# Kernel optimization log

Hardware: AMD Instinct MI355X
Metric: run time of the kernel (lower is better)

Reference implementation:

```python
import jax, jax.numpy as jnp
import numpy as np
import math

B, S, D, H, NF = 2, 2048, 1024, 16, 4
DH = D // H


def setup_inputs() -> dict:
    key = jax.random.key(0)
    ks = jax.random.split(key, 8)
    scale = 0.01 / math.sqrt(D)  # rough attenuated-kaiming scale for projections
    return {
        "x": jax.random.normal(ks[0], (B, S, D), dtype=jnp.float32),
        "weights": jax.random.uniform(ks[1], (1, NF), dtype=jnp.float32),
        "Wq": jax.random.normal(ks[2], (D, D), dtype=jnp.float32) * scale,
        "bq": jnp.zeros((D,), dtype=jnp.float32),
        "Wk": jax.random.normal(ks[3], (D, D), dtype=jnp.float32) * scale,
        "bk": jnp.zeros((D,), dtype=jnp.float32),
        "Wv": jax.random.normal(ks[4], (D, D), dtype=jnp.float32) * scale,
        "bv": jnp.zeros((D,), dtype=jnp.float32),
        "Wout": jax.random.normal(ks[5], (NF, D, D), dtype=jnp.float32) / math.sqrt(D),
        "bout": jnp.zeros((NF, D), dtype=jnp.float32),
    }


def reference(x, weights, Wq, bq, Wk, bk, Wv, bv, Wout, bout):
    # projections (torch Linear: x @ W.T + b)
    q = x @ Wq.T + bq  # [B,S,D]
    k = x @ Wk.T + bk
    v = x @ Wv.T + bv
    # split heads -> [B,H,S,DH]
    split = lambda t: t.reshape(B, S, H, DH).transpose(0, 2, 1, 3)
    q, k, v = split(q), split(k), split(v)
    # scores with causal additive mask of -10000 (as in get_attention_mask)
    scores = jnp.einsum("bhqd,bhkd->bhqk", q, k) / math.sqrt(DH)
    i = jnp.arange(S)
    causal = (i[None, :] <= i[:, None])  # [S,S] True where allowed
    mask = (1.0 - causal.astype(scores.dtype)) * -10000.0
    attn = jax.nn.softmax(scores + mask, axis=-1)
    # dropout is disabled (p=0.0)
    out = jnp.einsum("bhqk,bhkd->bhqd", attn, v)  # [B,H,S,DH]
    out = out.transpose(0, 2, 1, 3).reshape(B, S, D)
    # WeightedFunctions: per-function Linear(d,d) combined by weights[0]
    w0 = weights[0]  # [NF]
    Weff = jnp.einsum("f,fod->od", w0, Wout)  # [D,D]
    beff = w0 @ bout  # [D]
    return out @ Weff.T + beff
```

## Files before the change

### kernel.cpp

```cpp
#include <hip/hip_runtime.h>

typedef unsigned short u16;
typedef __bf16 bf16_t;
typedef bf16_t bf16x8 __attribute__((ext_vector_type(8)));
typedef bf16_t bf16x4 __attribute__((ext_vector_type(4)));
typedef float f32x4 __attribute__((ext_vector_type(4)));
typedef u16 u16x8 __attribute__((ext_vector_type(8)));
typedef u16 u16x4 __attribute__((ext_vector_type(4)));

#define DEV __device__ __forceinline__

DEV u16 f2bf(float f) {
  unsigned u = __float_as_uint(f);
  u += 0x7FFFu + ((u >> 16) & 1u);
  return (u16)(u >> 16);
}

DEV void async_ld16(const void* g, void* lds_wave_uniform) {
  __builtin_amdgcn_global_load_lds(
      (const __attribute__((address_space(1))) void*)g,
      (__attribute__((address_space(3))) void*)lds_wave_uniform, 16, 0, 0);
}

DEV int KF(int r) { return (r & 3) ^ ((r >> 2) & 1); }

__global__ __launch_bounds__(256) void prep_kernel(
    const float* __restrict__ x, const float* __restrict__ Wq,
    const float* __restrict__ Wk, const float* __restrict__ Wv,
    const float* __restrict__ w4, const float* __restrict__ Wout,
    const float* __restrict__ bout, u16* __restrict__ xbf,
    u16* __restrict__ wqkv, u16* __restrict__ Weff, float* __restrict__ beff) {
  constexpr int NX = 1048576;
  constexpr int NW = 262144;
  const int stride = gridDim.x * 256;
  for (int id = blockIdx.x * 256 + threadIdx.x; id < NX + 3 * NW + NW;
       id += stride) {
    if (id < NX) {
      const float4 v = ((const float4*)x)[id];
      u16x4 o;
      o[0] = f2bf(v.x); o[1] = f2bf(v.y); o[2] = f2bf(v.z); o[3] = f2bf(v.w);
      ((u16x4*)xbf)[id] = o;
    } else if (id < NX + 3 * NW) {
      const int wi = id - NX;
      const int which = wi >> 18, j = wi & (NW - 1);
      const float* src = which == 0 ? Wq : (which == 1 ? Wk : Wv);
      const float4 v = ((const float4*)src)[j];
      u16x4 o;
      o[0] = f2bf(v.x); o[1] = f2bf(v.y); o[2] = f2bf(v.z); o[3] = f2bf(v.w);
      ((u16x4*)wqkv)[wi] = o;
    } else {
      const int i = id - NX - 3 * NW;
      const float w0 = w4[0], w1 = w4[1], w2 = w4[2], w3 = w4[3];
      const float4* W = (const float4*)Wout;
      const float4 a = W[i], b1 = W[NW + i], b2 = W[2 * NW + i],
                   b3 = W[3 * NW + i];
      u16x4 o;
      o[0] = f2bf(w0 * a.x + w1 * b1.x + w2 * b2.x + w3 * b3.x);
      o[1] = f2bf(w0 * a.y + w1 * b1.y + w2 * b2.y + w3 * b3.y);
      o[2] = f2bf(w0 * a.z + w1 * b1.z + w2 * b2.z + w3 * b3.z);
      o[3] = f2bf(w0 * a.w + w1 * b1.w + w2 * b2.w + w3 * b3.w);
      ((u16x4*)Weff)[i] = o;
      if (i < 256) {
        const float4* B4 = (const float4*)bout;
        const float4 ba = B4[i], c1 = B4[256 + i], c2 = B4[512 + i],
                     c3 = B4[768 + i];
        float4 ob;
        ob.x = w0 * ba.x + w1 * c1.x + w2 * c2.x + w3 * c3.x;
        ob.y = w0 * ba.y + w1 * c1.y + w2 * c2.y + w3 * c3.y;
        ob.z = w0 * ba.z + w1 * c1.z + w2 * c2.z + w3 * c3.z;
        ob.w = w0 * ba.w + w1 * c1.w + w2 * c2.w + w3 * c3.w;
        ((float4*)beff)[i] = ob;
      }
    }
  }
}

#define GEMM_PIPELINE_LOOP(A_, B_, m0_, n0_, K_)                               \
  int rA[2], oA[2], dstc[2];                                                   \
  _Pragma("unroll") for (int j = 0; j < 2; ++j) {                              \
    const int c = (j * 4 + w) * 64 + lane;                                     \
    rA[j] = c >> 2;                                                            \
    oA[j] = ((c & 3) ^ KF(rA[j])) * 8;                                         \
    dstc[j] = (j * 4 + w) * 512;                                               \
  }                                                                            \
  auto stage = [&](int buf, int kt) {                                          \
    _Pragma("unroll") for (int j = 0; j < 2; ++j) {                            \
      async_ld16(A_ + (m0_ + rA[j]) * K_ + kt + oA[j],                         \
                 &LDS[buf * 4096 + dstc[j]]);                                  \
      async_ld16(B_ + (n0_ + rA[j]) * K_ + kt + oA[j],                         \
                 &LDS[12288 + buf * 4096 + dstc[j]]);                          \
    }                                                                          \
  };                                                                           \
  f32x4 acc[4][4] = {};                                                        \
  stage(0, 0);                                                                 \
  stage(1, 32);                                                                \
  const int nt = K_ / 32;                                                      \
  int cur = 0, stg = 2;                                                        \
  for (int t = 0; t < nt; ++t) {                                               \
    if (t == nt - 1)                                                           \
      asm volatile("s_waitcnt vmcnt(0)\ns_barrier" ::: "memory");              \
    else                                                                       \
      asm volatile("s_waitcnt vmcnt(4)\ns_barrier" ::: "memory");              \
    __builtin_amdgcn_sched_barrier(0);                                         \
    if (t + 2 < nt) stage(stg, (t + 2) * 32);                                  \
    bf16x8 af[4], bfr[4];                                                      \
    _Pragma("unroll") for (int i = 0; i < 4; ++i) {                            \
      const int ra = wr * 64 + i * 16 + l15;                                   \
      const int rb = wc * 64 + i * 16 + l15;                                   \
      af[i] = *(const bf16x8*)&LDS[cur * 4096 + ra * 32 + ((l4 ^ KF(ra)) * 8)];\
      bfr[i] = *(const bf16x8*)&LDS[12288 + cur * 4096 + rb * 32 +             \
                                    ((l4 ^ KF(rb)) * 8)];                      \
    }                                                                          \
    asm volatile("s_waitcnt lgkmcnt(0)" ::: "memory");                         \
    __builtin_amdgcn_sched_barrier(0);                                         \
    __builtin_amdgcn_s_setprio(1);                                             \
    _Pragma("unroll") for (int i = 0; i < 4; ++i)                              \
        _Pragma("unroll") for (int j = 0; j < 4; ++j)                          \
            acc[i][j] = __builtin_amdgcn_mfma_f32_16x16x32_bf16(               \
                af[i], bfr[j], acc[i][j], 0, 0, 0);                            \
    __builtin_amdgcn_s_setprio(0);                                             \
    cur = cur == 2 ? 0 : cur + 1;                                              \
    stg = stg == 2 ? 0 : stg + 1;                                              \
  }

__global__ __launch_bounds__(256) void gemm_bt_kernel(
    const u16* __restrict__ A, const u16* __restrict__ Bw,
    const float* __restrict__ bias, float* __restrict__ C, int M, int N, int K) {
  __shared__ u16 LDS[24576];
  const int tid = threadIdx.x;
  const int w = tid >> 6, lane = tid & 63;
  const int l15 = lane & 15, l4 = lane >> 4;
  const int wr = w >> 1, wc = w & 1;
  const long m0 = (long)blockIdx.y * 128, n0 = (long)blockIdx.x * 128;

  GEMM_PIPELINE_LOOP(A, Bw, m0, n0, K)

#pragma unroll
  for (int i = 0; i < 4; ++i) {
    const long row0 = m0 + wr * 64 + i * 16 + l4 * 4;
#pragma unroll
    for (int j = 0; j < 4; ++j) {
      const long col = n0 + wc * 64 + j * 16 + l15;
      const float bb = bias[col];
#pragma unroll
      for (int r = 0; r < 4; ++r)
        C[(row0 + r) * N + col] = acc[i][j][r] + bb;
    }
  }
}

__global__ __launch_bounds__(256) void gemm_qkv_kernel(
    const u16* __restrict__ A, const u16* __restrict__ Bw,
    const float* __restrict__ bq, const float* __restrict__ bk,
    const float* __restrict__ bv, u16* __restrict__ qo, u16* __restrict__ ko,
    u16* __restrict__ vt) {
  constexpr int K = 1024;
  __shared__ u16 LDS[24576];
  const int tid = threadIdx.x;
  const int w = tid >> 6, lane = tid & 63;
  const int l15 = lane & 15, l4 = lane >> 4;
  const int wr = w >> 1, wc = w & 1;
  const long m0 = (long)blockIdx.y * 128, n0 = (long)blockIdx.x * 128;
  const int seg = blockIdx.x >> 3;
  const float* bias = seg == 0 ? bq : (seg == 1 ? bk : bv);
  const float scale = seg == 0 ? 0.18033688011112042f : 1.0f;

  GEMM_PIPELINE_LOOP(A, Bw, m0, n0, K)

  __syncthreads();
  const long ccol0 = n0 - (long)seg * 1024;
  if (seg < 2) {
    u16* outp = seg == 0 ? qo : ko;
#pragma unroll
    for (int i = 0; i < 4; ++i) {
#pragma unroll
      for (int j = 0; j < 4; ++j) {
        const int colb = wc * 64 + j * 16 + l15;
        const float bb = bias[ccol0 + colb];
#pragma unroll
        for (int r = 0; r < 4; ++r) {
          const int row = wr * 64 + i * 16 + l4 * 4 + r;
          LDS[row * 128 + (colb ^ ((row & 15) << 3))] =
              f2bf((acc[i][j][r] + bb) * scale);
        }
      }
    }
    __syncthreads();
#pragma unroll
    for (int p = 0; p < 8; ++p) {
      const int cid = p * 256 + tid;
      const int row = cid >> 4, c = cid & 15;
      const u16x8 vch = *(const u16x8*)&LDS[row * 128 + ((c ^ (row & 15)) * 8)];
      *(u16x8*)&outp[(m0 + row) * 1024 + ccol0 + c * 8] = vch;
    }
  } else {
    const int b = (int)(m0 >> 11);
    const int s0 = (int)(m0 & 2047);
#pragma unroll
    for (int i = 0; i < 4; ++i) {
#pragma unroll
      for (int j = 0; j < 4; ++j) {
        const int colb = wc * 64 + j * 16 + l15;
        const float bb = bias[ccol0 + colb];
#pragma unroll
        for (int r = 0; r < 4; ++r) {
          const int row = wr * 64 + i * 16 + l4 * 4 + r;
          LDS[colb * 128 + (row ^ ((colb & 15) << 3))] = f2bf(acc[i][j][r] + bb);
        }
      }
    }
    __syncthreads();
#pragma unroll
    for (int p = 0; p < 8; ++p) {
      const int cid = p * 256 + tid;
      const int c = cid >> 4, r0 = (cid & 15) * 8;
      const u16x8 vch = *(const u16x8*)&LDS[c * 128 + (r0 ^ ((c & 15) << 3))];
      const int gcol = (int)ccol0 + c;
      const int h = gcol >> 6, d = gcol & 63;
      *(u16x8*)&vt[(size_t)((b * 16 + h) * 64 + d) * 2048 + s0 + r0] = vch;
    }
  }
}

__global__ __launch_bounds__(512) void flash_kernel(
    const u16* __restrict__ Q, const u16* __restrict__ Kg,
    const u16* __restrict__ Vt, u16* __restrict__ O,
    u16* __restrict__ accP, float* __restrict__ mP, float* __restrict__ lP) {
  constexpr int S = 2048, D = 1024, DH = 64;
  __shared__ u16 Ks[3][4096];
  __shared__ u16 Vs[3][4096];
  __shared__ u16 Ps[8][2048];
  const int tid = threadIdx.x;
  const int w = tid >> 6, lane = tid & 63;
  const int l15 = lane & 15, l4 = lane >> 4;
  const int bh = blockIdx.x, b = bh >> 4, h = bh & 15;
  const int xb = blockIdx.y;
  const int p = xb >> 1, seg = xb & 1;
  const int p1len = seg ? 0 : 4 * p + 4;
  const int kvoff = seg ? (14 - 4 * p) : 0;
  const int TA = seg ? (7 - p) : p;
  const int TB = 7 - p;
  const int qbA_keep = TA * 256 + w * 32;

  const u16* Kbh = Kg + (size_t)b * S * D + h * DH;
  const u16* Vbh = Vt + (size_t)bh * DH * S;

  const int srow = tid >> 3;
  const int scol = ((tid & 7) ^ (srow & 7)) * 8;
  const int sw = l15 & 7;

  bf16x8 qf[2][2], qfB[2][2];
#pragma unroll
  for (int c = 0; c < 2; ++c) {
    const u16* qp =
        Q + (size_t)(b * S + qbA_keep + c * 16 + l15) * D + h * DH + l4 * 8;
    qf[c][0] = *(const bf16x8*)qp;
    qf[c][1] = *(const bf16x8*)(qp + 32);
    qfB[c][0] = qf[c][0];
    qfB[c][1] = qf[c][1];
  }
  if (!seg) {
    const int qbB = TB * 256 + w * 32;
#pragma unroll
    for (int c = 0; c < 2; ++c) {
      const u16* qp =
          Q + (size_t)(b * S + qbB + c * 16 + l15) * D + h * DH + l4 * 8;
      qfB[c][0] = *(const bf16x8*)qp;
      qfB[c][1] = *(const bf16x8*)(qp + 32);
    }
  }

  f32x4 acc_o[2][4] = {};
  float m_run[2] = {-3e38f, -3e38f};
  float l_run[2] = {0.f, 0.f};

  int qb = qbA_keep;
  int qt64w = TA * 4 + (w >> 1);

  auto kv_of = [&](int j) { return (j < p1len) ? j : (j - p1len + kvoff); };
  auto stage = [&](int kv, int buf) {
    async_ld16(Kbh + (size_t)(kv * 64 + srow) * D + scol, &Ks[buf][w * 512]);
    async_ld16(Vbh + (size_t)srow * S + kv * 64 + scol, &Vs[buf][w * 512]);
  };

  stage(kv_of(0), 0);
  stage(kv_of(1), 1);

  constexpr int NST = 18;
  for (int j = 0; j < NST; ++j) {
    if (j == NST - 1)
      asm volatile("s_waitcnt vmcnt(0)\ns_barrier" ::: "memory");
    else
      asm volatile("s_waitcnt vmcnt(2)\ns_barrier" ::: "memory");
    __builtin_amdgcn_sched_barrier(0);
    if (j + 2 < NST) stage(kv_of(j + 2), (j + 2) % 3);

    if (seg == 0 && j == p1len) {
      float lt[2], lq[2][4];
#pragma unroll
      for (int c = 0; c < 2; ++c) {
        float t = l_run[c];
        t += __shfl_xor(t, 16);
        t += __shfl_xor(t, 32);
        lt[c] = t;
#pragma unroll
        for (int r = 0; r < 4; ++r) lq[c][r] = __shfl(lt[c], l4 * 4 + r, 64);
      }
#pragma unroll
      for (int c = 0; c < 2; ++c)
#pragma unroll
        for (int db = 0; db < 4; ++db)
#pragma unroll
          for (int r = 0; r < 4; ++r) {
            const int row = c * 16 + l4 * 4 + r;
            const int col = db * 16 + l15;
            Ps[w][row * 64 + (col ^ ((row & 7) << 3))] =
                f2bf(acc_o[c][db][r] / lq[c][r]);
          }
      asm volatile("s_waitcnt lgkmcnt(0)" ::: "memory");
#pragma unroll
      for (int j4 = 0; j4 < 4; ++j4) {
        const int cid = j4 * 64 + lane;
        const int row = cid >> 3, c8 = cid & 7;
        const u16x8 vch =
            *(const u16x8*)&Ps[w][row * 64 + ((c8 ^ (row & 7)) * 8)];
        *(u16x8*)&O[(size_t)(b * S + qbA_keep + row) * D + h * DH + c8 * 8] =
            vch;
      }
#pragma unroll
      for (int c = 0; c < 2; ++c) {
        qf[c][0] = qfB[c][0];
        qf[c][1] = qfB[c][1];
        m_run[c] = -3e38f;
        l_run[c] = 0.f;
#pragma unroll
        for (int db = 0; db < 4; ++db) acc_o[c][db] = f32x4{0.f, 0.f, 0.f, 0.f};
      }
      qb = TB * 256 + w * 32;
      qt64w = TB * 4 + (w >> 1);
    }

    const int it = kv_of(j);
    const int buf = j % 3;
    if (it <= qt64w) {
      f32x4 accs[2][4] = {};
      __builtin_amdgcn_s_setprio(1);
#pragma unroll
      for (int cb = 0; cb < 4; ++cb) {
        const int row = cb * 16 + l15;
        const bf16x8 kf0 = *(const bf16x8*)&Ks[buf][row * 64 + ((l4 ^ sw) * 8)];
        const bf16x8 kf1 =
            *(const bf16x8*)&Ks[buf][row * 64 + (((l4 + 4) ^ sw) * 8)];
#pragma unroll
        for (int c = 0; c < 2; ++c) {
          accs[c][cb] = __builtin_amdgcn_mfma_f32_16x16x32_bf16(
              kf0, qf[c][0], accs[c][cb], 0, 0, 0);
          accs[c][cb] = __builtin_amdgcn_mfma_f32_16x16x32_bf16(
              kf1, qf[c][1], accs[c][cb], 0, 0, 0);
        }
      }
      __builtin_amdgcn_s_setprio(0);
      bf16x8 vf0[4], vf1[4];
#pragma unroll
      for (int db = 0; db < 4; ++db) {
        const int row = db * 16 + l15;
        vf0[db] = *(const bf16x8*)&Vs[buf][row * 64 + ((l4 ^ sw) * 8)];
        vf1[db] = *(const bf16x8*)&Vs[buf][row * 64 + (((l4 + 4) ^ sw) * 8)];
      }
      float mx[2] = {-3e38f, -3e38f};
      if (it == qt64w) {
#pragma unroll
        for (int c = 0; c < 2; ++c)
#pragma unroll
          for (int cb = 0; cb < 4; ++cb)
#pragma unroll
            for (int r = 0; r < 4; ++r) {
              float s_ = accs[c][cb][r];
              if (it * 64 + cb * 16 + l4 * 4 + r > qb + c * 16 + l15)
                s_ = -3e38f;
              accs[c][cb][r] = s_;
              mx[c] = fmaxf(mx[c], s_);
            }
      } else {
#pragma unroll
        for (int c = 0; c < 2; ++c)
#pragma unroll
          for (int cb = 0; cb < 4; ++cb)
#pragma unroll
            for (int r = 0; r < 4; ++r) mx[c] = fmaxf(mx[c], accs[c][cb][r]);
      }
      if (!__all(fmaxf(mx[0] - m_run[0], mx[1] - m_run[1]) <= 8.0f)) {
#pragma unroll
        for (int c = 0; c < 2; ++c) {
          float m = mx[c];
          m = fmaxf(m, __shfl_xor(m, 16));
          m = fmaxf(m, __shfl_xor(m, 32));
          const float mn = fmaxf(m_run[c], m);
          const float corr = __builtin_amdgcn_exp2f(m_run[c] - mn);
          m_run[c] = mn;
          float cq[4];
#pragma unroll
          for (int r = 0; r < 4; ++r) cq[r] = __shfl(corr, l4 * 4 + r, 64);
#pragma unroll
          for (int db = 0; db < 4; ++db)
#pragma unroll
            for (int r = 0; r < 4; ++r) acc_o[c][db][r] *= cq[r];
          l_run[c] *= corr;
        }
      }
#pragma unroll
      for (int c = 0; c < 2; ++c) {
        float rs = 0.f;
#pragma unroll
        for (int cb = 0; cb < 4; ++cb)
#pragma unroll
          for (int r = 0; r < 4; ++r) {
            const float pv = __builtin_amdgcn_exp2f(accs[c][cb][r] - m_run[c]);
            accs[c][cb][r] = pv;
            rs += pv;
          }
        l_run[c] += rs;
      }
#pragma unroll
      for (int c = 0; c < 2; ++c)
#pragma unroll
        for (int cb = 0; cb < 4; ++cb) {
          bf16x4 pk = {(bf16_t)accs[c][cb][0], (bf16_t)accs[c][cb][1],
                       (bf16_t)accs[c][cb][2], (bf16_t)accs[c][cb][3]};
          const int chunk = (2 * cb + (l4 >> 1)) ^ sw;
          *(bf16x4*)&Ps[w][(c * 16 + l15) * 64 + chunk * 8 + (l4 & 1) * 4] = pk;
        }
      asm volatile("s_waitcnt lgkmcnt(0)" ::: "memory");
      bf16x8 pa[2][2];
#pragma unroll
      for (int c = 0; c < 2; ++c)
#pragma unroll
        for (int mf = 0; mf < 2; ++mf) {
          const int chunk = (mf * 4 + l4) ^ sw;
          pa[c][mf] =
              *(const bf16x8*)&Ps[w][(c * 16 + l15) * 64 + chunk * 8];
        }
      __builtin_amdgcn_s_setprio(1);
#pragma unroll
      for (int db = 0; db < 4; ++db) {
#pragma unroll
        for (int c = 0; c < 2; ++c) {
          acc_o[c][db] = __builtin_amdgcn_mfma_f32_16x16x32_bf16(
              pa[c][0], vf0[db], acc_o[c][db], 0, 0, 0);
          acc_o[c][db] = __builtin_amdgcn_mfma_f32_16x16x32_bf16(
              pa[c][1], vf1[db], acc_o[c][db], 0, 0, 0);
        }
      }
      __builtin_amdgcn_s_setprio(0);
    }
  }

  float lt[2];
#pragma unroll
  for (int c = 0; c < 2; ++c) {
    float t = l_run[c];
    t += __shfl_xor(t, 16);
    t += __shfl_xor(t, 32);
    lt[c] = t;
  }
#pragma unroll
  for (int c = 0; c < 2; ++c)
#pragma unroll
    for (int db = 0; db < 4; ++db)
#pragma unroll
      for (int r = 0; r < 4; ++r) {
        const int row = c * 16 + l4 * 4 + r;
        const int col = db * 16 + l15;
        Ps[w][row * 64 + (col ^ ((row & 7) << 3))] = f2bf(acc_o[c][db][r]);
      }
  asm volatile("s_waitcnt lgkmcnt(0)" ::: "memory");
  const size_t base =
      (size_t)seg * 32768 + (size_t)bh * 1024 + (TB * 256 + w * 32 - 1024);
#pragma unroll
  for (int j4 = 0; j4 < 4; ++j4) {
    const int cid = j4 * 64 + lane;
    const int row = cid >> 3, c8 = cid & 7;
    const u16x8 vch = *(const u16x8*)&Ps[w][row * 64 + ((c8 ^ (row & 7)) * 8)];
    *(u16x8*)&accP[(base + row) * 64 + c8 * 8] = vch;
  }
  if (l4 == 0) {
#pragma unroll
    for (int c = 0; c < 2; ++c) {
      mP[base + c * 16 + l15] = m_run[c];
      lP[base + c * 16 + l15] = lt[c];
    }
  }
}

__global__ __launch_bounds__(256) void combine_kernel(
    const u16* __restrict__ accP, const float* __restrict__ mP,
    const float* __restrict__ lP, u16* __restrict__ O) {
  const int id = blockIdx.x * 256 + threadIdx.x;
  const int row = id >> 3;
  const int c0 = (id & 7) * 8;
  const float m0 = mP[row], m1 = mP[32768 + row];
  const float l0 = lP[row], l1 = lP[32768 + row];
  const float M = fmaxf(m0, m1);
  const float e0 = __builtin_amdgcn_exp2f(m0 - M);
  const float e1 = __builtin_amdgcn_exp2f(m1 - M);
  const float inv = 1.f / (l0 * e0 + l1 * e1);
  const bf16_t* aP = (const bf16_t*)accP;
  const bf16x8 a0 = *(const bf16x8*)&aP[(size_t)row * 64 + c0];
  const bf16x8 a1 = *(const bf16x8*)&aP[(size_t)(32768 + row) * 64 + c0];
  const int bh = row >> 10, s = 1024 + (row & 1023);
  const int b = bh >> 4, h = bh & 15;
  bf16_t* out = (bf16_t*)O + (size_t)(b * 2048 + s) * 1024 + h * 64 + c0;
  bf16x8 o;
#pragma unroll
  for (int j = 0; j < 8; ++j)
    o[j] = (bf16_t)(((float)a0[j] * e0 + (float)a1[j] * e1) * inv);
  *(bf16x8*)out = o;
}

extern "C" void kernel_launch(void* const* d_in, const int* in_sizes, int n_in,
                              void* d_out, int out_size, void* d_ws, size_t ws_size,
                              hipStream_t stream) {
  (void)in_sizes; (void)n_in; (void)out_size;
  const float* x   = (const float*)d_in[0];
  const float* wts = (const float*)d_in[1];
  const float* Wq  = (const float*)d_in[2];
  const float* bq  = (const float*)d_in[3];
  const float* Wk  = (const float*)d_in[4];
  const float* bk  = (const float*)d_in[5];
  const float* Wv  = (const float*)d_in[6];
  const float* bv  = (const float*)d_in[7];
  const float* Wo  = (const float*)d_in[8];
  const float* bo  = (const float*)d_in[9];
  float* out = (float*)d_out;

  if (ws_size < 58724352) return;

  char* ws = (char*)d_ws;
  u16* xbf  = (u16*)(ws + 0);
  u16* qbf  = (u16*)(ws + 8388608);
  u16* kbf  = (u16*)(ws + 16777216);
  u16* vt   = (u16*)(ws + 33554432);
  u16* attn = (u16*)(ws + 41943040);
  u16* wqkv = (u16*)(ws + 50331648);
  u16* wob  = (u16*)(ws + 56623104);
  float* beff = (float*)(ws + 58720256);

  u16* accP = xbf;
  float* mP = (float*)(ws + 50331648);
  float* lP = mP + 65536;

  prep_kernel<<<2048, 256, 0, stream>>>(x, Wq, Wk, Wv, wts, Wo, bo,
                                        xbf, wqkv, wob, beff);
  gemm_qkv_kernel<<<dim3(24, 32), 256, 0, stream>>>(xbf, wqkv, bq, bk, bv,
                                                    qbf, kbf, vt);
  flash_kernel<<<dim3(32, 8), 512, 0, stream>>>(qbf, kbf, vt, attn,
                                                accP, mP, lP);
  combine_kernel<<<1024, 256, 0, stream>>>(accP, mP, lP, attn);
  gemm_bt_kernel<<<dim3(8, 32), 256, 0, stream>>>(
      attn, wob, beff, out, 4096, 1024, 1024);
}
```

Before: 104.8 us.

## Enlarge QKV GEMM tile to 256x256 with 512 threads and 3-stage pipeline

```diff
diff --git a/kernel.cpp b/kernel.cpp
--- a/kernel.cpp
+++ b/kernel.cpp
@@ -149,75 +149,141 @@
   }
 }
 
-__global__ __launch_bounds__(256) void gemm_qkv_kernel(
+__global__ __launch_bounds__(512) void gemm_qkv_kernel(
     const u16* __restrict__ A, const u16* __restrict__ Bw,
     const float* __restrict__ bq, const float* __restrict__ bk,
     const float* __restrict__ bv, u16* __restrict__ qo, u16* __restrict__ ko,
     u16* __restrict__ vt) {
   constexpr int K = 1024;
-  __shared__ u16 LDS[24576];
+  __shared__ u16 LDS[49152];
   const int tid = threadIdx.x;
   const int w = tid >> 6, lane = tid & 63;
   const int l15 = lane & 15, l4 = lane >> 4;
-  const int wr = w >> 1, wc = w & 1;
-  const long m0 = (long)blockIdx.y * 128, n0 = (long)blockIdx.x * 128;
-  const int seg = blockIdx.x >> 3;
+  const int wr = w >> 2, wc = w & 3;
+  const long m0 = (long)blockIdx.y * 256, n0 = (long)blockIdx.x * 256;
+  const int seg = blockIdx.x >> 2;
   const float* bias = seg == 0 ? bq : (seg == 1 ? bk : bv);
   const float scale = seg == 0 ? 0.18033688011112042f : 1.0f;
 
-  GEMM_PIPELINE_LOOP(A, Bw, m0, n0, K)
+  int rA[2], oA[2], dstc[2];
+#pragma unroll
+  for (int j = 0; j < 2; ++j) {
+    const int c = (j * 8 + w) * 64 + lane;
+    rA[j] = c >> 2;
+    oA[j] = ((c & 3) ^ KF(rA[j])) * 8;
+    dstc[j] = (j * 8 + w) * 512;
+  }
+  auto stage = [&](int buf, int kt) {
+#pragma unroll
+    for (int j = 0; j < 2; ++j) {
+      async_ld16(A + (m0 + rA[j]) * K + kt + oA[j],
+                 &LDS[buf * 8192 + dstc[j]]);
+      async_ld16(Bw + (n0 + rA[j]) * K + kt + oA[j],
+                 &LDS[24576 + buf * 8192 + dstc[j]]);
+    }
+  };
+
+  f32x4 acc[8][4] = {};
+  stage(0, 0);
+  stage(1, 32);
+  const int nt = K / 32;
+  int cur = 0, stg = 2;
+  for (int t = 0; t < nt; ++t) {
+    if (t == nt - 1)
+      asm volatile("s_waitcnt vmcnt(0)\ns_barrier" ::: "memory");
+    else
+      asm volatile("s_waitcnt vmcnt(4)\ns_barrier" ::: "memory");
+    __builtin_amdgcn_sched_barrier(0);
+    if (t + 2 < nt) stage(stg, (t + 2) * 32);
+    bf16x8 af[8], bfr[4];
+#pragma unroll
+    for (int i = 0; i < 8; ++i) {
+      const int ra = wr * 128 + i * 16 + l15;
+      af[i] = *(const bf16x8*)&LDS[cur * 8192 + ra * 32 + ((l4 ^ KF(ra)) * 8)];
+    }
+#pragma unroll
+    for (int j = 0; j < 4; ++j) {
+      const int rb = wc * 64 + j * 16 + l15;
+      bfr[j] = *(const bf16x8*)&LDS[24576 + cur * 8192 + rb * 32 +
+                                    ((l4 ^ KF(rb)) * 8)];
+    }
+    asm volatile("s_waitcnt lgkmcnt(0)" ::: "memory");
+    __builtin_amdgcn_sched_barrier(0);
+    __builtin_amdgcn_s_setprio(1);
+#pragma unroll
+    for (int i = 0; i < 8; ++i)
+#pragma unroll
+      for (int j = 0; j < 4; ++j)
+        acc[i][j] = __builtin_amdgcn_mfma_f32_16x16x32_bf16(af[i], bfr[j],
+                                                            acc[i][j], 0, 0, 0);
+    __builtin_amdgcn_s_setprio(0);
+    cur = cur == 2 ? 0 : cur + 1;
+    stg = stg == 2 ? 0 : stg + 1;
+  }
 
   __syncthreads();
   const long ccol0 = n0 - (long)seg * 1024;
   if (seg < 2) {
     u16* outp = seg == 0 ? qo : ko;
 #pragma unroll
-    for (int i = 0; i < 4; ++i) {
-#pragma unroll
-      for (int j = 0; j < 4; ++j) {
-        const int colb = wc * 64 + j * 16 + l15;
-        const float bb = bias[ccol0 + colb];
-#pragma unroll
-        for (int r = 0; r < 4; ++r) {
-          const int row = wr * 64 + i * 16 + l4 * 4 + r;
-          LDS[row * 128 + (colb ^ ((row & 15) << 3))] =
-              f2bf((acc[i][j][r] + bb) * scale);
-        }
-      }
-    }
-    __syncthreads();
-#pragma unroll
-    for (int p = 0; p < 8; ++p) {
-      const int cid = p * 256 + tid;
-      const int row = cid >> 4, c = cid & 15;
-      const u16x8 vch = *(const u16x8*)&LDS[row * 128 + ((c ^ (row & 15)) * 8)];
-      *(u16x8*)&outp[(m0 + row) * 1024 + ccol0 + c * 8] = vch;
+    for (int h = 0; h < 2; ++h) {
+      if ((wc >> 1) == h) {
+#pragma unroll
+        for (int i = 0; i < 8; ++i)
+#pragma unroll
+          for (int j = 0; j < 4; ++j) {
+            const int colb = (wc & 1) * 64 + j * 16 + l15;
+            const float bb = bias[ccol0 + h * 128 + colb];
+#pragma unroll
+            for (int r = 0; r < 4; ++r) {
+              const int row = wr * 128 + i * 16 + l4 * 4 + r;
+              LDS[row * 128 + (colb ^ ((row & 15) << 3))] =
+                  f2bf((acc[i][j][r] + bb) * scale);
+            }
+          }
+      }
+      __syncthreads();
+#pragma unroll
+      for (int p = 0; p < 8; ++p) {
+        const int cid = p * 512 + tid;
+        const int row = cid >> 4, c = cid & 15;
+        const u16x8 vch =
+            *(const u16x8*)&LDS[row * 128 + ((c ^ (row & 15)) * 8)];
+        *(u16x8*)&outp[(m0 + row) * 1024 + ccol0 + h * 128 + c * 8] = vch;
+      }
+      __syncthreads();
     }
   } else {
     const int b = (int)(m0 >> 11);
     const int s0 = (int)(m0 & 2047);
 #pragma unroll
-    for (int i = 0; i < 4; ++i) {
-#pragma unroll
-      for (int j = 0; j < 4; ++j) {
-        const int colb = wc * 64 + j * 16 + l15;
-        const float bb = bias[ccol0 + colb];
-#pragma unroll
-        for (int r = 0; r < 4; ++r) {
-          const int row = wr * 64 + i * 16 + l4 * 4 + r;
-          LDS[colb * 128 + (row ^ ((colb & 15) << 3))] = f2bf(acc[i][j][r] + bb);
-        }
-      }
-    }
-    __syncthreads();
-#pragma unroll
-    for (int p = 0; p < 8; ++p) {
-      const int cid = p * 256 + tid;
-      const int c = cid >> 4, r0 = (cid & 15) * 8;
-      const u16x8 vch = *(const u16x8*)&LDS[c * 128 + (r0 ^ ((c & 15) << 3))];
-      const int gcol = (int)ccol0 + c;
-      const int h = gcol >> 6, d = gcol & 63;
-      *(u16x8*)&vt[(size_t)((b * 16 + h) * 64 + d) * 2048 + s0 + r0] = vch;
+    for (int h = 0; h < 2; ++h) {
+      if ((wc >> 1) == h) {
+#pragma unroll
+        for (int i = 0; i < 8; ++i)
+#pragma unroll
+          for (int j = 0; j < 4; ++j) {
+            const int colb = (wc & 1) * 64 + j * 16 + l15;
+            const float bb = bias[ccol0 + h * 128 + colb];
+#pragma unroll
+            for (int r = 0; r < 4; ++r) {
+              const int row = wr * 128 + i * 16 + l4 * 4 + r;
+              LDS[colb * 256 + (row ^ ((colb & 15) << 3))] =
+                  f2bf(acc[i][j][r] + bb);
+            }
+          }
+      }
+      __syncthreads();
+#pragma unroll
+      for (int p = 0; p < 8; ++p) {
+        const int cid = p * 512 + tid;
+        const int c = cid >> 5, r0 = (cid & 31) * 8;
+        const u16x8 vch = *(const u16x8*)&LDS[c * 256 + (r0 ^ ((c & 15) << 3))];
+        const int gcol = (int)ccol0 + h * 128 + c;
+        const int hh = gcol >> 6, d = gcol & 63;
+        *(u16x8*)&vt[(size_t)((b * 16 + hh) * 64 + d) * 2048 + s0 + r0] = vch;
+      }
+      __syncthreads();
     }
   }
 }
@@ -551,7 +617,7 @@
 
   prep_kernel<<<2048, 256, 0, stream>>>(x, Wq, Wk, Wv, wts, Wo, bo,
                                         xbf, wqkv, wob, beff);
-  gemm_qkv_kernel<<<dim3(24, 32), 256, 0, stream>>>(xbf, wqkv, bq, bk, bv,
+  gemm_qkv_kernel<<<dim3(12, 16), 512, 0, stream>>>(xbf, wqkv, bq, bk, bv,
                                                     qbf, kbf, vt);
   flash_kernel<<<dim3(32, 8), 512, 0, stream>>>(qbf, kbf, vt, attn,
                                                 accP, mP, lP);
```

After: 108.0 us. 3.1% more time.
